# Performance work log

Hardware: AMD Instinct MI355X
Metric: run time of the kernel (lower is better)

The kernel has to match this reference:

```python
import jax, jax.numpy as jnp
import numpy as np

B, S, IN = 32, 512, 19
DE, DD = 256, 128      # encoder / decoder d_model
HE, HD = 8, 4          # heads
LE, LD = 6, 2          # layers
FE, FD = 4 * DE, 4 * DD
EPS = 1e-5


def _ln(x, g, b):
    m = x.mean(-1, keepdims=True)
    v = ((x - m) ** 2).mean(-1, keepdims=True)
    return (x - m) / jnp.sqrt(v + EPS) * g + b


def _mha(x, qkv_w, qkv_b, out_w, out_b, kpad, nh):
    Bq, Sq, D = x.shape
    dh = D // nh
    qkv = x @ qkv_w.T + qkv_b
    q, k, v = jnp.split(qkv, 3, axis=-1)
    hs = lambda t: t.reshape(Bq, Sq, nh, dh).transpose(0, 2, 1, 3)  # -> [B,h,S,dh]
    q, k, v = hs(q), hs(k), hs(v)
    scores = jnp.einsum('bhqd,bhkd->bhqk', q, k) / float(np.sqrt(dh))
    scores = jnp.where(kpad[:, None, None, :], -1e9, scores)  # mask padded keys
    attn = jax.nn.softmax(scores, axis=-1)
    o = jnp.einsum('bhqk,bhkd->bhqd', attn, v).transpose(0, 2, 1, 3).reshape(Bq, Sq, D)
    return o @ out_w.T + out_b


def _block(x, p, kpad, nh):
    qkv_w, qkv_b, ow, ob, f1w, f1b, f2w, f2b, g1, b1, g2, b2 = p
    x = _ln(x + _mha(x, qkv_w, qkv_b, ow, ob, kpad, nh), g1, b1)
    h = jax.nn.relu(x @ f1w.T + f1b) @ f2w.T + f2b
    return _ln(x + h, g2, b2)


def _run(x, ps, kpad, nh, L):
    for i in range(L):
        x = _block(x, tuple(p[i] for p in ps), kpad, nh)
    return x


def _forward(event_tensor, w_in_enc, b_in_enc,
             enc_qkv_w, enc_qkv_b, enc_out_w, enc_out_b,
             enc_f1_w, enc_f1_b, enc_f2_w, enc_f2_b,
             enc_g1, enc_b1, enc_g2, enc_b2,
             mask_token, e2d_w,
             dec_qkv_w, dec_qkv_b, dec_out_w, dec_out_b,
             dec_f1_w, dec_f1_b, dec_f2_w, dec_f2_b,
             dec_g1, dec_b1, dec_g2, dec_b2,
             qh_w, qh_b, dth_w, dth_b,
             attention_mask, pred_mask):
    visible = attention_mask & (~pred_mask)
    counts = visible.sum(axis=1)                                  # [B]
    order = jnp.argsort(~visible, axis=1, stable=True)            # visible positions packed first, in order
    tok = event_tensor @ w_in_enc.T + b_in_enc                    # [B,S,DE]
    vis = jnp.take_along_axis(tok, order[:, :, None], axis=1)
    pos = jnp.arange(S)
    enc_pad = pos[None, :] >= counts[:, None]                      # True = padded slot
    vis = jnp.where(enc_pad[:, :, None], 0.0, vis)
    enc_ps = (enc_qkv_w, enc_qkv_b, enc_out_w, enc_out_b, enc_f1_w, enc_f1_b,
              enc_f2_w, enc_f2_b, enc_g1, enc_b1, enc_g2, enc_b2)
    enc_out = _run(vis, enc_ps, enc_pad, HE, LE)
    dec_vis = enc_out @ e2d_w.T                                    # [B,S,DD]
    idx = jnp.cumsum(visible.astype(jnp.int32), axis=1) - 1        # position -> packed index
    gathered = jnp.take_along_axis(dec_vis, jnp.clip(idx, 0)[:, :, None], axis=1)
    dec_in = jnp.where(visible[:, :, None], gathered, mask_token)  # mask token at masked/pad slots
    dec_ps = (dec_qkv_w, dec_qkv_b, dec_out_w, dec_out_b, dec_f1_w, dec_f1_b,
              dec_f2_w, dec_f2_b, dec_g1, dec_b1, dec_g2, dec_b2)
    dec_out = _run(dec_in, dec_ps, ~attention_mask, HD, LD)
    q = dec_out @ qh_w.T + qh_b
    dt = dec_out @ dth_w.T + dth_b
    return jnp.concatenate([q, dt], axis=-1)                       # [B,S,2]


def setup_inputs():
    key = jax.random.key(0)
    ks = iter(jax.random.split(key, 64))
    nrm = lambda shp, s=0.02: jax.random.normal(next(ks), shp, jnp.float32) * s
    d = {}
    d['event_tensor'] = jax.random.normal(next(ks), (B, S, IN), jnp.float32)
    lengths = jax.random.randint(next(ks), (B,), S // 2, S + 1)
    pos = jnp.arange(S)
    am = pos[None, :] < lengths[:, None]
    pm = (jax.random.uniform(next(ks), (B, S)) < 0.75) & am
    pm = pm.at[:, 0].set(False)  # guarantee >=1 visible token per row
    d['attention_mask'] = am
    d['pred_mask'] = pm
    d['w_in_enc'] = nrm((DE, IN)); d['b_in_enc'] = jnp.zeros((DE,), jnp.float32)
    d['enc_qkv_w'] = nrm((LE, 3 * DE, DE)); d['enc_qkv_b'] = jnp.zeros((LE, 3 * DE), jnp.float32)
    d['enc_out_w'] = nrm((LE, DE, DE));     d['enc_out_b'] = jnp.zeros((LE, DE), jnp.float32)
    d['enc_f1_w'] = nrm((LE, FE, DE));      d['enc_f1_b'] = jnp.zeros((LE, FE), jnp.float32)
    d['enc_f2_w'] = nrm((LE, DE, FE));      d['enc_f2_b'] = jnp.zeros((LE, DE), jnp.float32)
    d['enc_g1'] = jnp.ones((LE, DE), jnp.float32); d['enc_b1'] = jnp.zeros((LE, DE), jnp.float32)
    d['enc_g2'] = jnp.ones((LE, DE), jnp.float32); d['enc_b2'] = jnp.zeros((LE, DE), jnp.float32)
    d['mask_token'] = nrm((DD,))
    d['e2d_w'] = nrm((DD, DE))
    d['dec_qkv_w'] = nrm((LD, 3 * DD, DD)); d['dec_qkv_b'] = jnp.zeros((LD, 3 * DD), jnp.float32)
    d['dec_out_w'] = nrm((LD, DD, DD));     d['dec_out_b'] = jnp.zeros((LD, DD), jnp.float32)
    d['dec_f1_w'] = nrm((LD, FD, DD));      d['dec_f1_b'] = jnp.zeros((LD, FD), jnp.float32)
    d['dec_f2_w'] = nrm((LD, DD, FD));      d['dec_f2_b'] = jnp.zeros((LD, DD), jnp.float32)
    d['dec_g1'] = jnp.ones((LD, DD), jnp.float32); d['dec_b1'] = jnp.zeros((LD, DD), jnp.float32)
    d['dec_g2'] = jnp.ones((LD, DD), jnp.float32); d['dec_b2'] = jnp.zeros((LD, DD), jnp.float32)
    d['qh_w'] = nrm((1, DD));  d['qh_b'] = jnp.zeros((1,), jnp.float32)
    d['dth_w'] = nrm((1, DD)); d['dth_b'] = jnp.zeros((1,), jnp.float32)
    return d


def reference(event_tensor, attention_mask, pred_mask, w_in_enc, b_in_enc,
              enc_qkv_w, enc_qkv_b, enc_out_w, enc_out_b,
              enc_f1_w, enc_f1_b, enc_f2_w, enc_f2_b,
              enc_g1, enc_b1, enc_g2, enc_b2,
              mask_token, e2d_w,
              dec_qkv_w, dec_qkv_b, dec_out_w, dec_out_b,
              dec_f1_w, dec_f1_b, dec_f2_w, dec_f2_b,
              dec_g1, dec_b1, dec_g2, dec_b2,
              qh_w, qh_b, dth_w, dth_b):
    return _forward(event_tensor, w_in_enc, b_in_enc,
                    enc_qkv_w, enc_qkv_b, enc_out_w, enc_out_b,
                    enc_f1_w, enc_f1_b, enc_f2_w, enc_f2_b,
                    enc_g1, enc_b1, enc_g2, enc_b2,
                    mask_token, e2d_w,
                    dec_qkv_w, dec_qkv_b, dec_out_w, dec_out_b,
                    dec_f1_w, dec_f1_b, dec_f2_w, dec_f2_b,
                    dec_g1, dec_b1, dec_g2, dec_b2,
                    qh_w, qh_b, dth_w, dth_b,
                    attention_mask, pred_mask)
```

## Files before the change

### kernel.cpp

```cpp
#include <hip/hip_runtime.h>
#include <hip/hip_bf16.h>

#define B_ 32
#define S_ 512
#define IN_ 19
#define DE_ 256
#define DD_ 128
#define HE_ 8
#define HD_ 4
#define LE_ 6
#define LD_ 2
#define FE_ 1024
#define FD_ 512
#define DH_ 32

typedef __attribute__((ext_vector_type(8))) short short8;
typedef __attribute__((ext_vector_type(4))) float f32x4;

__device__ __forceinline__ short f2bf(float f) {
    union { float f; unsigned u; } x; x.f = f;
    unsigned r = x.u + 0x7fff + ((x.u >> 16) & 1);
    return (short)(r >> 16);
}
__device__ __forceinline__ float bf2f(short s) {
    union { unsigned u; float f; } x; x.u = ((unsigned)(unsigned short)s) << 16;
    return x.f;
}

#define GLL16(g, l) __builtin_amdgcn_global_load_lds( \
    (const __attribute__((address_space(1))) void*)(g), \
    (__attribute__((address_space(3))) void*)(l), 16, 0, 0)

#define QSCALE 0.2550653169f

#define NCONV 9
struct ConvTab {
    const float* src[NCONV];
    short* dst[NCONV];
    int len[NCONV];
};
__global__ __launch_bounds__(S_) void conv_plan_kernel(
    ConvTab tab, int total,
    const int* __restrict__ am, const int* __restrict__ pm,
    int* __restrict__ counts, int* __restrict__ lengths, int* __restrict__ order,
    int* __restrict__ visible, int* __restrict__ idx) {
    if (blockIdx.x < B_) {
        int b = blockIdx.x, s = threadIdx.x;
        __shared__ int sc[S_];
        int a = (am[b * S_ + s] != 0);
        int v = a && (pm[b * S_ + s] == 0);
        visible[b * S_ + s] = v;
        sc[s] = v | (a << 16);
        __syncthreads();
#pragma unroll
        for (int off = 1; off < S_; off <<= 1) {
            int t = (s >= off) ? sc[s - off] : 0;
            __syncthreads();
            sc[s] += t;
            __syncthreads();
        }
        int incl = sc[s] & 0xffff;
        int tot = sc[S_ - 1];
        int total2 = tot & 0xffff;
        if (s == 0) { counts[b] = total2; lengths[b] = tot >> 16; }
        idx[b * S_ + s] = (incl > 0) ? incl - 1 : 0;
        if (v) order[b * S_ + incl - 1] = s;
        else   order[b * S_ + total2 + (s - incl)] = s;
    } else {
        int i = (blockIdx.x - B_) * S_ + threadIdx.x;
        if (i >= total) return;
        int j = i;
        for (int e = 0; e < NCONV; ++e) {
            if (j < tab.len[e]) { tab.dst[e][j] = f2bf(tab.src[e][j]); return; }
            j -= tab.len[e];
        }
    }
}

__global__ __launch_bounds__(DE_) void enc_embed_kernel(
    const float* __restrict__ ev, const float* __restrict__ w, const float* __restrict__ bias,
    const int* __restrict__ counts, const int* __restrict__ order, short* __restrict__ out) {
    int bs = blockIdx.x;
    int b = bs / S_, s = bs % S_;
    int d = threadIdx.x;
    __shared__ float e[IN_];
    bool padded = (s >= counts[b]);
    int src = order[bs];
    if (threadIdx.x < IN_)
        e[threadIdx.x] = padded ? 0.f : ev[(size_t)(b * S_ + src) * IN_ + threadIdx.x];
    __syncthreads();
    float acc = bias[d];
#pragma unroll
    for (int i = 0; i < IN_; ++i) acc += e[i] * w[d * IN_ + i];
    out[(size_t)bs * DE_ + d] = padded ? f2bf(0.f) : f2bf(acc);
}

template <int TM, int TN, bool RELU, bool QKV>
__global__ __launch_bounds__(256) void gemm_mfma(
    const short* __restrict__ A, const short* __restrict__ Wt, const float* __restrict__ bias,
    short* __restrict__ C, int M, int N, int K,
    short* __restrict__ qb, short* __restrict__ kb, short* __restrict__ vtb, int H, int D,
    const int* __restrict__ live) {
    constexpr int HM = TM / 2, HN = TN / 2;
    constexpr int MI = HM / 16, NI = HN / 16;
    constexpr int NCHA = TM / 16, NCH = (TM + TN) / 16;
    int bm = blockIdx.y * TM, bn = blockIdx.x * TN;
    if (live && (bm & (S_ - 1)) >= live[bm >> 9]) return;
    __shared__ short As[2][TM][32];
    __shared__ short Bs[2][TN][32];
    int t = threadIdx.x;
    int wave = t >> 6, lane = t & 63;
    int wm = (wave >> 1) * HM, wn = (wave & 1) * HN;
    int c = lane & 15, quad = lane >> 4;
    f32x4 acc[MI][NI];
#pragma unroll
    for (int i = 0; i < MI; ++i)
#pragma unroll
        for (int j = 0; j < NI; ++j) acc[i][j] = (f32x4){0.f, 0.f, 0.f, 0.f};

    int srow = lane >> 2, scol = (lane & 3) * 8;
    int nk = K >> 5;

    auto stage = [&](int buf, int k0) {
#pragma unroll
        for (int ch0 = 0; ch0 < NCH; ch0 += 4) {
            int ch = ch0 + wave;
            if (ch < NCHA)
                GLL16(A + (size_t)(bm + ch * 16 + srow) * K + k0 + scol, &As[buf][ch * 16][0]);
            else if (ch < NCH)
                GLL16(Wt + (size_t)(bn + (ch - NCHA) * 16 + srow) * K + k0 + scol,
                      &Bs[buf][(ch - NCHA) * 16][0]);
        }
    };

    stage(0, 0);
    __syncthreads();
    for (int kt = 0; kt < nk; ++kt) {
        int cur = kt & 1;
        if (kt + 1 < nk) stage(cur ^ 1, (kt + 1) << 5);
        short8 av[MI], bv[NI];
#pragma unroll
        for (int mi = 0; mi < MI; ++mi) av[mi] = *(const short8*)&As[cur][wm + mi * 16 + c][quad * 8];
#pragma unroll
        for (int ni = 0; ni < NI; ++ni) bv[ni] = *(const short8*)&Bs[cur][wn + ni * 16 + c][quad * 8];
#pragma unroll
        for (int mi = 0; mi < MI; ++mi)
#pragma unroll
            for (int ni = 0; ni < NI; ++ni)
                acc[mi][ni] = __builtin_amdgcn_mfma_f32_16x16x32_bf16(av[mi], bv[ni], acc[mi][ni], 0, 0, 0);
        __syncthreads();
    }
#pragma unroll
    for (int mi = 0; mi < MI; ++mi)
#pragma unroll
        for (int ni = 0; ni < NI; ++ni)
#pragma unroll
            for (int r = 0; r < 4; ++r) {
                int R = bm + wm + mi * 16 + quad * 4 + r;
                int Ncol = bn + wn + ni * 16 + c;
                float v = acc[mi][ni][r] + (bias ? bias[Ncol] : 0.f);
                if (RELU) v = fmaxf(v, 0.f);
                if (!QKV) {
                    C[(size_t)R * N + Ncol] = f2bf(v);
                } else {
                    int s = R & (S_ - 1), b2 = R >> 9;
                    if (Ncol < D) {
                        int h = Ncol >> 5, d = Ncol & 31;
                        qb[(((size_t)b2 * H + h) * S_ + s) * DH_ + d] = f2bf(v * QSCALE);
                    } else if (Ncol < 2 * D) {
                        int n2 = Ncol - D, h = n2 >> 5, d = n2 & 31;
                        kb[(((size_t)b2 * H + h) * S_ + s) * DH_ + d] = f2bf(v);
                    } else {
                        int n2 = Ncol - 2 * D, h = n2 >> 5, d = n2 & 31;
                        vtb[(((size_t)b2 * H + h) * DH_ + d) * S_ + s] = f2bf(v);
                    }
                }
            }
}

template <int N, bool HEAD>
__global__ __launch_bounds__(256) void gemm_ln(
    const short* __restrict__ A, const short* __restrict__ Wt,
    const float* __restrict__ bias, const short* x ,
    const float* __restrict__ g, const float* __restrict__ be,
    short* out,
    const float* __restrict__ qw, const float* __restrict__ qbb,
    const float* __restrict__ dw, const float* __restrict__ dbb,
    float* __restrict__ outf,
    int K, const int* __restrict__ live) {
    constexpr int TM = 32;
    constexpr int HN = N / 2, NI = HN / 16;
    constexpr int NCHA = TM / 16, NCH = NCHA + N / 16;
    constexpr int HST = N + 8;
    constexpr int BUF = (TM + N) * 32;
    int bm = blockIdx.x * TM;
    if (live && (bm & (S_ - 1)) >= live[bm >> 9]) return;
    __shared__ short smem[2 * BUF];
    int t = threadIdx.x, wave = t >> 6, lane = t & 63;
    int wm = (wave >> 1) * 16, wn = (wave & 1) * HN;
    int c = lane & 15, quad = lane >> 4;
    int srow = lane >> 2, scol = (lane & 3) * 8;
    f32x4 acc[NI];
#pragma unroll
    for (int ni = 0; ni < NI; ++ni) acc[ni] = (f32x4){0.f, 0.f, 0.f, 0.f};
    int nk = K >> 5;

    auto stage = [&](int buf, int k0) {
        short* base = smem + buf * BUF;
#pragma unroll
        for (int ch0 = 0; ch0 < NCH; ch0 += 4) {
            int ch = ch0 + wave;
            if (ch < NCHA)
                GLL16(A + (size_t)(bm + ch * 16 + srow) * K + k0 + scol, base + ch * 16 * 32);
            else if (ch < NCH)
                GLL16(Wt + (size_t)((ch - NCHA) * 16 + srow) * K + k0 + scol,
                      base + (TM + (ch - NCHA) * 16) * 32);
        }
    };

    stage(0, 0);
    __syncthreads();
    for (int kt = 0; kt < nk; ++kt) {
        int cur = kt & 1;
        if (kt + 1 < nk) stage(cur ^ 1, (kt + 1) << 5);
        const short* base = smem + cur * BUF;
        short8 av = *(const short8*)(base + (wm + c) * 32 + quad * 8);
        short8 bv[NI];
#pragma unroll
        for (int ni = 0; ni < NI; ++ni)
            bv[ni] = *(const short8*)(base + (TM + wn + ni * 16 + c) * 32 + quad * 8);
#pragma unroll
        for (int ni = 0; ni < NI; ++ni)
            acc[ni] = __builtin_amdgcn_mfma_f32_16x16x32_bf16(av, bv[ni], acc[ni], 0, 0, 0);
        __syncthreads();
    }

    short* Hs = smem;
#pragma unroll
    for (int ni = 0; ni < NI; ++ni) {
        int col = wn + ni * 16 + c;
        float bcol = bias[col];
#pragma unroll
        for (int r = 0; r < 4; ++r)
            Hs[(wm + quad * 4 + r) * HST + col] = f2bf(acc[ni][r] + bcol);
    }
    __syncthreads();

    constexpr int CPL = N / 8;
    int r = t >> 3, li = t & 7;
    int R = bm + r;
    int c0 = li * CPL;
    float v[CPL];
    float s = 0.f;
#pragma unroll
    for (int e8 = 0; e8 < CPL / 8; ++e8) {
        short8 xv = *(const short8*)&x[(size_t)R * N + c0 + e8 * 8];
#pragma unroll
        for (int j = 0; j < 8; ++j) {
            float vv = bf2f(xv[j]) + bf2f(Hs[r * HST + c0 + e8 * 8 + j]);
            v[e8 * 8 + j] = vv;
            s += vv;
        }
    }
    s += __shfl_xor(s, 1); s += __shfl_xor(s, 2); s += __shfl_xor(s, 4);
    float m = s / N;
    float s2 = 0.f;
#pragma unroll
    for (int e = 0; e < CPL; ++e) { float d = v[e] - m; s2 += d * d; }
    s2 += __shfl_xor(s2, 1); s2 += __shfl_xor(s2, 2); s2 += __shfl_xor(s2, 4);
    float rstd = rsqrtf(s2 / N + 1e-5f);
    if (!HEAD) {
        if (live && ((R & (S_ - 1)) >= live[R >> 9])) return;
#pragma unroll
        for (int e8 = 0; e8 < CPL / 8; ++e8) {
            short8 ov;
#pragma unroll
            for (int j = 0; j < 8; ++j) {
                int e = e8 * 8 + j;
                ov[j] = f2bf((v[e] - m) * rstd * g[c0 + e] + be[c0 + e]);
            }
            *(short8*)&out[(size_t)R * N + c0 + e8 * 8] = ov;
        }
    } else {
        float q = 0.f, dt = 0.f;
#pragma unroll
        for (int e = 0; e < CPL; ++e) {
            float o = (v[e] - m) * rstd * g[c0 + e] + be[c0 + e];
            q += o * qw[c0 + e];
            dt += o * dw[c0 + e];
        }
        q += __shfl_xor(q, 1); q += __shfl_xor(q, 2); q += __shfl_xor(q, 4);
        dt += __shfl_xor(dt, 1); dt += __shfl_xor(dt, 2); dt += __shfl_xor(dt, 4);
        if (li == 0) {
            outf[(size_t)R * 2 + 0] = q + qbb[0];
            outf[(size_t)R * 2 + 1] = dt + dbb[0];
        }
    }
}

__global__ __launch_bounds__(256) void attn_flash(
    const short* __restrict__ qb, const short* __restrict__ kb, const short* __restrict__ vtb,
    const int* __restrict__ limit_arr, const int* __restrict__ qlim,
    short* __restrict__ o, int H, int D) {
    int b = blockIdx.z, h = blockIdx.y;
    if (qlim && (int)(blockIdx.x * 64) >= qlim[b]) return;
    int wave = threadIdx.x >> 6, lane = threadIdx.x & 63;
    int q0 = blockIdx.x * 64 + wave * 16;
    int c = lane & 15, quad = lane >> 4;
    size_t bh = (size_t)b * H + h;
    __shared__ short PtAll[4][16][132];
    short (*Pt)[132] = PtAll[wave];

    f32x4 zero = (f32x4){0.f, 0.f, 0.f, 0.f};
    short8 aq = *(const short8*)&qb[(bh * S_ + q0 + c) * DH_ + quad * 8];
    const short* kbase = kb + bh * S_ * DH_;
    const short* vbase = vtb + bh * DH_ * S_;

    int limit = limit_arr[b];
    int nchunks = (limit + 127) >> 7;

    float lrow[4] = {0.f, 0.f, 0.f, 0.f};
    f32x4 o0 = zero, o1 = zero;

    for (int kc = 0; kc < nchunks; ++kc) {
        f32x4 s[8];
#pragma unroll
        for (int nt = 0; nt < 8; ++nt) {
            short8 bk = *(const short8*)&kbase[(size_t)(kc * 128 + nt * 16 + c) * DH_ + quad * 8];
            s[nt] = __builtin_amdgcn_mfma_f32_16x16x32_bf16(aq, bk, zero, 0, 0, 0);
        }
#pragma unroll
        for (int nt = 0; nt < 8; ++nt) {
            bool ok = (kc * 128 + nt * 16 + c) < limit;
#pragma unroll
            for (int r = 0; r < 4; ++r) {
                float p = ok ? exp2f(s[nt][r]) : 0.f;
                s[nt][r] = p;
                lrow[r] += p;
            }
        }
#pragma unroll
        for (int nt = 0; nt < 8; ++nt)
#pragma unroll
            for (int r = 0; r < 4; ++r)
                Pt[quad * 4 + r][nt * 16 + c] = f2bf(s[nt][r]);
#pragma unroll
        for (int kk = 0; kk < 4; ++kk) {
            short8 ap = *(const short8*)&Pt[c][kk * 32 + quad * 8];
            short8 b0 = *(const short8*)&vbase[(size_t)c * S_ + kc * 128 + kk * 32 + quad * 8];
            short8 b1 = *(const short8*)&vbase[(size_t)(16 + c) * S_ + kc * 128 + kk * 32 + quad * 8];
            o0 = __builtin_amdgcn_mfma_f32_16x16x32_bf16(ap, b0, o0, 0, 0, 0);
            o1 = __builtin_amdgcn_mfma_f32_16x16x32_bf16(ap, b1, o1, 0, 0, 0);
        }
    }
#pragma unroll
    for (int r = 0; r < 4; ++r) {
        float l = lrow[r];
        l += __shfl_xor(l, 1);
        l += __shfl_xor(l, 2);
        l += __shfl_xor(l, 4);
        l += __shfl_xor(l, 8);
        float inv = 1.f / l;
        int row = quad * 4 + r;
        size_t base = (size_t)(b * S_ + q0 + row) * D + h * DH_;
        o[base + c] = f2bf(o0[r] * inv);
        o[base + 16 + c] = f2bf(o1[r] * inv);
    }
}

__global__ __launch_bounds__(DD_) void dec_embed_kernel(
    const short* __restrict__ dec_vis, const float* __restrict__ mask_token,
    const int* __restrict__ visible, const int* __restrict__ idx, short* __restrict__ out) {
    int bs = blockIdx.x, d = threadIdx.x;
    int b = bs / S_;
    short val = visible[bs] ? dec_vis[(size_t)(b * S_ + idx[bs]) * DD_ + d]
                            : f2bf(mask_token[d]);
    out[(size_t)bs * DD_ + d] = val;
}

extern "C" void kernel_launch(void* const* d_in, const int* in_sizes, int n_in,
                              void* d_out, int out_size, void* d_ws, size_t ws_size,
                              hipStream_t stream) {
    const float* ev      = (const float*)d_in[0];
    const int*  am       = (const int*)d_in[1];
    const int*  pm       = (const int*)d_in[2];
    const float* w_in    = (const float*)d_in[3];
    const float* b_in    = (const float*)d_in[4];
    const float* eqkv_w  = (const float*)d_in[5];
    const float* eqkv_b  = (const float*)d_in[6];
    const float* eout_w  = (const float*)d_in[7];
    const float* eout_b  = (const float*)d_in[8];
    const float* ef1_w   = (const float*)d_in[9];
    const float* ef1_b   = (const float*)d_in[10];
    const float* ef2_w   = (const float*)d_in[11];
    const float* ef2_b   = (const float*)d_in[12];
    const float* eg1     = (const float*)d_in[13];
    const float* eb1     = (const float*)d_in[14];
    const float* eg2     = (const float*)d_in[15];
    const float* eb2     = (const float*)d_in[16];
    const float* mask_tok= (const float*)d_in[17];
    const float* e2d_w   = (const float*)d_in[18];
    const float* dqkv_w  = (const float*)d_in[19];
    const float* dqkv_b  = (const float*)d_in[20];
    const float* dout_w  = (const float*)d_in[21];
    const float* dout_b  = (const float*)d_in[22];
    const float* df1_w   = (const float*)d_in[23];
    const float* df1_b   = (const float*)d_in[24];
    const float* df2_w   = (const float*)d_in[25];
    const float* df2_b   = (const float*)d_in[26];
    const float* dg1     = (const float*)d_in[27];
    const float* db1     = (const float*)d_in[28];
    const float* dg2     = (const float*)d_in[29];
    const float* db2     = (const float*)d_in[30];
    const float* qh_w    = (const float*)d_in[31];
    const float* qh_b    = (const float*)d_in[32];
    const float* dth_w   = (const float*)d_in[33];
    const float* dth_b   = (const float*)d_in[34];
    float* out = (float*)d_out;

    const int BS = B_ * S_;
    char* ws = (char*)d_ws;
    int* counts  = (int*)ws;
    int* lengths = counts + 32;
    int* order   = lengths + 32;
    int* visible = order + BS;
    int* idx     = visible + BS;

    short* wb = (short*)(ws + 256 * 1024);
    const int L_eqkv = LE_ * 3 * DE_ * DE_;
    const int L_eout = LE_ * DE_ * DE_;
    const int L_ef1  = LE_ * FE_ * DE_;
    const int L_ef2  = LE_ * DE_ * FE_;
    const int L_e2d  = DD_ * DE_;
    const int L_dqkv = LD_ * 3 * DD_ * DD_;
    const int L_dout = LD_ * DD_ * DD_;
    const int L_df1  = LD_ * FD_ * DD_;
    const int L_df2  = LD_ * DD_ * FD_;
    short* w_eqkv = wb;
    short* w_eout = w_eqkv + L_eqkv;
    short* w_ef1  = w_eout + L_eout;
    short* w_ef2  = w_ef1 + L_ef1;
    short* w_e2d  = w_ef2 + L_ef2;
    short* w_dqkv = w_e2d + L_e2d;
    short* w_dout = w_dqkv + L_dqkv;
    short* w_df1  = w_dout + L_dout;
    short* w_df2  = w_df1 + L_df1;
    const int convTotal = L_eqkv + L_eout + L_ef1 + L_ef2 + L_e2d + L_dqkv + L_dout + L_df1 + L_df2;

    short* bx    = (short*)(ws + 12 * 1024 * 1024);
    short* qbuf  = bx   + (size_t)BS * DE_;
    short* kbuf  = qbuf + (size_t)B_ * HE_ * S_ * DH_;
    short* vtbuf = kbuf + (size_t)B_ * HE_ * S_ * DH_;
    short* battn = vtbuf + (size_t)B_ * HE_ * S_ * DH_;
    short* bt    = battn + (size_t)BS * DE_;
    short* hid   = bt + (size_t)BS * DE_;

    ConvTab tab;
    tab.src[0] = eqkv_w; tab.dst[0] = w_eqkv; tab.len[0] = L_eqkv;
    tab.src[1] = eout_w; tab.dst[1] = w_eout; tab.len[1] = L_eout;
    tab.src[2] = ef1_w;  tab.dst[2] = w_ef1;  tab.len[2] = L_ef1;
    tab.src[3] = ef2_w;  tab.dst[3] = w_ef2;  tab.len[3] = L_ef2;
    tab.src[4] = e2d_w;  tab.dst[4] = w_e2d;  tab.len[4] = L_e2d;
    tab.src[5] = dqkv_w; tab.dst[5] = w_dqkv; tab.len[5] = L_dqkv;
    tab.src[6] = dout_w; tab.dst[6] = w_dout; tab.len[6] = L_dout;
    tab.src[7] = df1_w;  tab.dst[7] = w_df1;  tab.len[7] = L_df1;
    tab.src[8] = df2_w;  tab.dst[8] = w_df2;  tab.len[8] = L_df2;
    conv_plan_kernel<<<B_ + (convTotal + S_ - 1) / S_, S_, 0, stream>>>(
        tab, convTotal, am, pm, counts, lengths, order, visible, idx);
    enc_embed_kernel<<<BS, DE_, 0, stream>>>(ev, w_in, b_in, counts, order, bx);

    for (int l = 0; l < LE_; ++l) {
        gemm_mfma<64, 64, false, true><<<dim3(3 * DE_ / 64, BS / 64), 256, 0, stream>>>(
            bx, w_eqkv + (size_t)l * 3 * DE_ * DE_, eqkv_b + (size_t)l * 3 * DE_,
            nullptr, BS, 3 * DE_, DE_, qbuf, kbuf, vtbuf, HE_, DE_, counts);
        attn_flash<<<dim3(S_ / 64, HE_, B_), 256, 0, stream>>>(
            qbuf, kbuf, vtbuf, counts, counts, battn, HE_, DE_);
        gemm_ln<DE_, false><<<BS / 32, 256, 0, stream>>>(
            battn, w_eout + (size_t)l * DE_ * DE_, eout_b + (size_t)l * DE_,
            bx, eg1 + (size_t)l * DE_, eb1 + (size_t)l * DE_, bx,
            nullptr, nullptr, nullptr, nullptr, nullptr, DE_, counts);
        gemm_mfma<64, 64, true, false><<<dim3(FE_ / 64, BS / 64), 256, 0, stream>>>(
            bx, w_ef1 + (size_t)l * FE_ * DE_, ef1_b + (size_t)l * FE_,
            hid, BS, FE_, DE_, nullptr, nullptr, nullptr, 0, 0, counts);
        gemm_ln<DE_, false><<<BS / 32, 256, 0, stream>>>(
            hid, w_ef2 + (size_t)l * DE_ * FE_, ef2_b + (size_t)l * DE_,
            bx, eg2 + (size_t)l * DE_, eb2 + (size_t)l * DE_, bx,
            nullptr, nullptr, nullptr, nullptr, nullptr, FE_, counts);
    }

    gemm_mfma<32, 32, false, false><<<dim3(DD_ / 32, BS / 32), 256, 0, stream>>>(
        bx, w_e2d, nullptr, bt, BS, DD_, DE_, nullptr, nullptr, nullptr, 0, 0, counts);
    dec_embed_kernel<<<BS, DD_, 0, stream>>>(bt, mask_tok, visible, idx, bx);

    for (int l = 0; l < LD_; ++l) {
        gemm_mfma<64, 64, false, true><<<dim3(3 * DD_ / 64, BS / 64), 256, 0, stream>>>(
            bx, w_dqkv + (size_t)l * 3 * DD_ * DD_, dqkv_b + (size_t)l * 3 * DD_, nullptr,
            BS, 3 * DD_, DD_, qbuf, kbuf, vtbuf, HD_, DD_, nullptr);
        attn_flash<<<dim3(S_ / 64, HD_, B_), 256, 0, stream>>>(
            qbuf, kbuf, vtbuf, lengths, nullptr, battn, HD_, DD_);
        gemm_ln<DD_, false><<<BS / 32, 256, 0, stream>>>(
            battn, w_dout + (size_t)l * DD_ * DD_, dout_b + (size_t)l * DD_,
            bx, dg1 + (size_t)l * DD_, db1 + (size_t)l * DD_, bx,
            nullptr, nullptr, nullptr, nullptr, nullptr, DD_, nullptr);
        gemm_mfma<64, 64, true, false><<<dim3(FD_ / 64, BS / 64), 256, 0, stream>>>(
            bx, w_df1 + (size_t)l * FD_ * DD_, df1_b + (size_t)l * FD_,
            hid, BS, FD_, DD_, nullptr, nullptr, nullptr, 0, 0, nullptr);
        if (l < LD_ - 1) {
            gemm_ln<DD_, false><<<BS / 32, 256, 0, stream>>>(
                hid, w_df2 + (size_t)l * DD_ * FD_, df2_b + (size_t)l * DD_,
                bx, dg2 + (size_t)l * DD_, db2 + (size_t)l * DD_, bx,
                nullptr, nullptr, nullptr, nullptr, nullptr, FD_, nullptr);
        } else {
            gemm_ln<DD_, true><<<BS / 32, 256, 0, stream>>>(
                hid, w_df2 + (size_t)l * DD_ * FD_, df2_b + (size_t)l * DD_,
                bx, dg2 + (size_t)l * DD_, db2 + (size_t)l * DD_, nullptr,
                qh_w, qh_b, dth_w, dth_b, out, FD_, nullptr);
        }
    }
}
```

Measured before the change: 855.6 us.

## Deepen GEMM global-to-LDS pipeline with explicit vmcnt waits and per-shape kernels

Replaces double buffering in the MFMA GEMM and GEMM+LayerNorm kernels with a 3-4 stage ring of LDS buffers. Each iteration waits only for the oldest tile using counted s_waitcnt vmcnt plus a single barrier, instead of a full syncthreads after every k-step. Kernels are also specialised into per-shape wrappers with compile-time N/K. The deeper prefetch is meant to hide global load latency, at the cost of more LDS per block and hand-counted wait logic that could be fragile.

```diff
diff --git a/kernel.cpp b/kernel.cpp
--- a/kernel.cpp
+++ b/kernel.cpp
@@ -30,6 +30,20 @@
 #define GLL16(g, l) __builtin_amdgcn_global_load_lds( \
     (const __attribute__((address_space(1))) void*)(g), \
     (__attribute__((address_space(3))) void*)(l), 16, 0, 0)
+
+__device__ __forceinline__ void waitvm(int n) {
+    switch (n) {
+    case 0: asm volatile("s_waitcnt vmcnt(0)" ::: "memory"); break;
+    case 1: asm volatile("s_waitcnt vmcnt(1)" ::: "memory"); break;
+    case 2: asm volatile("s_waitcnt vmcnt(2)" ::: "memory"); break;
+    case 3: asm volatile("s_waitcnt vmcnt(3)" ::: "memory"); break;
+    case 4: asm volatile("s_waitcnt vmcnt(4)" ::: "memory"); break;
+    default: asm volatile("s_waitcnt vmcnt(5)" ::: "memory"); break;
+    }
+}
+__device__ __forceinline__ void wait_lgkm0() {
+    asm volatile("s_waitcnt lgkmcnt(0)" ::: "memory");
+}
 
 #define QSCALE 0.2550653169f
 
@@ -95,10 +109,10 @@
     out[(size_t)bs * DE_ + d] = padded ? f2bf(0.f) : f2bf(acc);
 }
 
-template <int TM, int TN, bool RELU, bool QKV>
-__global__ __launch_bounds__(256) void gemm_mfma(
+template <int TM, int TN, bool RELU, bool QKV, int DEPTH>
+__device__ __forceinline__ void gemm_body(
     const short* __restrict__ A, const short* __restrict__ Wt, const float* __restrict__ bias,
-    short* __restrict__ C, int M, int N, int K,
+    short* __restrict__ C, int N, int K,
     short* __restrict__ qb, short* __restrict__ kb, short* __restrict__ vtb, int H, int D,
     const int* __restrict__ live) {
     constexpr int HM = TM / 2, HN = TN / 2;
@@ -106,8 +120,8 @@
     constexpr int NCHA = TM / 16, NCH = (TM + TN) / 16;
     int bm = blockIdx.y * TM, bn = blockIdx.x * TN;
     if (live && (bm & (S_ - 1)) >= live[bm >> 9]) return;
-    __shared__ short As[2][TM][32];
-    __shared__ short Bs[2][TN][32];
+    __shared__ short As[DEPTH][TM][32];
+    __shared__ short Bs[DEPTH][TN][32];
     int t = threadIdx.x;
     int wave = t >> 6, lane = t & 63;
     int wm = (wave >> 1) * HM, wn = (wave & 1) * HN;
@@ -119,9 +133,11 @@
         for (int j = 0; j < NI; ++j) acc[i][j] = (f32x4){0.f, 0.f, 0.f, 0.f};
 
     int srow = lane >> 2, scol = (lane & 3) * 8;
+    const int myloads = (NCH - wave + 3) >> 2;
     int nk = K >> 5;
 
-    auto stage = [&](int buf, int k0) {
+    auto stage = [&](int buf, int kt) {
+        int k0 = kt << 5;
 #pragma unroll
         for (int ch0 = 0; ch0 < NCH; ch0 += 4) {
             int ch = ch0 + wave;
@@ -133,11 +149,19 @@
         }
     };
 
-    stage(0, 0);
-    __syncthreads();
+#pragma unroll
+    for (int i = 0; i < DEPTH - 1; ++i)
+        if (i < nk) stage(i, i);
+
     for (int kt = 0; kt < nk; ++kt) {
-        int cur = kt & 1;
-        if (kt + 1 < nk) stage(cur ^ 1, (kt + 1) << 5);
+        int cur = kt % DEPTH;
+        int smax = (nk - 1 < kt + DEPTH - 2) ? nk - 1 : kt + DEPTH - 2;
+        waitvm((smax - kt) * myloads);
+        wait_lgkm0();
+        __builtin_amdgcn_s_barrier();
+        __builtin_amdgcn_sched_barrier(0);
+        int nxt = kt + DEPTH - 1;
+        if (nxt < nk) stage(nxt % DEPTH, nxt);
         short8 av[MI], bv[NI];
 #pragma unroll
         for (int mi = 0; mi < MI; ++mi) av[mi] = *(const short8*)&As[cur][wm + mi * 16 + c][quad * 8];
@@ -148,7 +172,6 @@
 #pragma unroll
             for (int ni = 0; ni < NI; ++ni)
                 acc[mi][ni] = __builtin_amdgcn_mfma_f32_16x16x32_bf16(av[mi], bv[ni], acc[mi][ni], 0, 0, 0);
-        __syncthreads();
     }
 #pragma unroll
     for (int mi = 0; mi < MI; ++mi)
@@ -179,7 +202,7 @@
 }
 
 template <int N, bool HEAD>
-__global__ __launch_bounds__(256) void gemm_ln(
+__device__ __forceinline__ void gemm_ln_body(
     const short* __restrict__ A, const short* __restrict__ Wt,
     const float* __restrict__ bias, const short* x ,
     const float* __restrict__ g, const float* __restrict__ be,
@@ -189,13 +212,14 @@
     float* __restrict__ outf,
     int K, const int* __restrict__ live) {
     constexpr int TM = 32;
+    constexpr int DEPTH = 3;
     constexpr int HN = N / 2, NI = HN / 16;
     constexpr int NCHA = TM / 16, NCH = NCHA + N / 16;
     constexpr int HST = N + 8;
     constexpr int BUF = (TM + N) * 32;
     int bm = blockIdx.x * TM;
     if (live && (bm & (S_ - 1)) >= live[bm >> 9]) return;
-    __shared__ short smem[2 * BUF];
+    __shared__ short smem[DEPTH * BUF];
     int t = threadIdx.x, wave = t >> 6, lane = t & 63;
     int wm = (wave >> 1) * 16, wn = (wave & 1) * HN;
     int c = lane & 15, quad = lane >> 4;
@@ -203,10 +227,12 @@
     f32x4 acc[NI];
 #pragma unroll
     for (int ni = 0; ni < NI; ++ni) acc[ni] = (f32x4){0.f, 0.f, 0.f, 0.f};
+    const int myloads = (NCH - wave + 3) >> 2;
     int nk = K >> 5;
 
-    auto stage = [&](int buf, int k0) {
+    auto stage = [&](int buf, int kt) {
         short* base = smem + buf * BUF;
+        int k0 = kt << 5;
 #pragma unroll
         for (int ch0 = 0; ch0 < NCH; ch0 += 4) {
             int ch = ch0 + wave;
@@ -218,11 +244,19 @@
         }
     };
 
-    stage(0, 0);
-    __syncthreads();
+#pragma unroll
+    for (int i = 0; i < DEPTH - 1; ++i)
+        if (i < nk) stage(i, i);
+
     for (int kt = 0; kt < nk; ++kt) {
-        int cur = kt & 1;
-        if (kt + 1 < nk) stage(cur ^ 1, (kt + 1) << 5);
+        int cur = kt % DEPTH;
+        int smax = (nk - 1 < kt + DEPTH - 2) ? nk - 1 : kt + DEPTH - 2;
+        waitvm((smax - kt) * myloads);
+        wait_lgkm0();
+        __builtin_amdgcn_s_barrier();
+        __builtin_amdgcn_sched_barrier(0);
+        int nxt = kt + DEPTH - 1;
+        if (nxt < nk) stage(nxt % DEPTH, nxt);
         const short* base = smem + cur * BUF;
         short8 av = *(const short8*)(base + (wm + c) * 32 + quad * 8);
         short8 bv[NI];
@@ -232,8 +266,8 @@
 #pragma unroll
         for (int ni = 0; ni < NI; ++ni)
             acc[ni] = __builtin_amdgcn_mfma_f32_16x16x32_bf16(av, bv[ni], acc[ni], 0, 0, 0);
-        __syncthreads();
-    }
+    }
+    __syncthreads();
 
     short* Hs = smem;
 #pragma unroll
@@ -296,6 +330,55 @@
             outf[(size_t)R * 2 + 1] = dt + dbb[0];
         }
     }
+}
+
+__global__ __launch_bounds__(256) void g_qkv_e(
+    const short* A, const short* Wt, const float* bias,
+    short* qb, short* kb, short* vtb, const int* live) {
+    gemm_body<64, 64, false, true, 4>(A, Wt, bias, nullptr, 3 * DE_, DE_, qb, kb, vtb, HE_, DE_, live);
+}
+__global__ __launch_bounds__(256) void g_qkv_d(
+    const short* A, const short* Wt, const float* bias,
+    short* qb, short* kb, short* vtb) {
+    gemm_body<64, 64, false, true, 4>(A, Wt, bias, nullptr, 3 * DD_, DD_, qb, kb, vtb, HD_, DD_, nullptr);
+}
+__global__ __launch_bounds__(256) void g_f1_e(
+    const short* A, const short* Wt, const float* bias, short* C, const int* live) {
+    gemm_body<64, 64, true, false, 4>(A, Wt, bias, C, FE_, DE_, nullptr, nullptr, nullptr, 0, 0, live);
+}
+__global__ __launch_bounds__(256) void g_f1_d(
+    const short* A, const short* Wt, const float* bias, short* C) {
+    gemm_body<64, 64, true, false, 4>(A, Wt, bias, C, FD_, DD_, nullptr, nullptr, nullptr, 0, 0, nullptr);
+}
+__global__ __launch_bounds__(256) void g_e2d(
+    const short* A, const short* Wt, short* C, const int* live) {
+    gemm_body<32, 32, false, false, 4>(A, Wt, nullptr, C, DD_, DE_, nullptr, nullptr, nullptr, 0, 0, live);
+}
+__global__ __launch_bounds__(256) void g_outln_e(
+    const short* A, const short* Wt, const float* bias, const short* x,
+    const float* g, const float* be, short* out, const int* live) {
+    gemm_ln_body<DE_, false>(A, Wt, bias, x, g, be, out, nullptr, nullptr, nullptr, nullptr, nullptr, DE_, live);
+}
+__global__ __launch_bounds__(256) void g_f2ln_e(
+    const short* A, const short* Wt, const float* bias, const short* x,
+    const float* g, const float* be, short* out, const int* live) {
+    gemm_ln_body<DE_, false>(A, Wt, bias, x, g, be, out, nullptr, nullptr, nullptr, nullptr, nullptr, FE_, live);
+}
+__global__ __launch_bounds__(256) void g_outln_d(
+    const short* A, const short* Wt, const float* bias, const short* x,
+    const float* g, const float* be, short* out) {
+    gemm_ln_body<DD_, false>(A, Wt, bias, x, g, be, out, nullptr, nullptr, nullptr, nullptr, nullptr, DD_, nullptr);
+}
+__global__ __launch_bounds__(256) void g_f2ln_d(
+    const short* A, const short* Wt, const float* bias, const short* x,
+    const float* g, const float* be, short* out) {
+    gemm_ln_body<DD_, false>(A, Wt, bias, x, g, be, out, nullptr, nullptr, nullptr, nullptr, nullptr, FD_, nullptr);
+}
+__global__ __launch_bounds__(256) void g_headln(
+    const short* A, const short* Wt, const float* bias, const short* x,
+    const float* g, const float* be,
+    const float* qw, const float* qbb, const float* dw, const float* dbb, float* outf) {
+    gemm_ln_body<DD_, true>(A, Wt, bias, x, g, be, nullptr, qw, qbb, dw, dbb, outf, FD_, nullptr);
 }
 
 __global__ __launch_bounds__(256) void attn_flash(
@@ -470,51 +553,44 @@
     enc_embed_kernel<<<BS, DE_, 0, stream>>>(ev, w_in, b_in, counts, order, bx);
 
     for (int l = 0; l < LE_; ++l) {
-        gemm_mfma<64, 64, false, true><<<dim3(3 * DE_ / 64, BS / 64), 256, 0, stream>>>(
+        g_qkv_e<<<dim3(3 * DE_ / 64, BS / 64), 256, 0, stream>>>(
             bx, w_eqkv + (size_t)l * 3 * DE_ * DE_, eqkv_b + (size_t)l * 3 * DE_,
-            nullptr, BS, 3 * DE_, DE_, qbuf, kbuf, vtbuf, HE_, DE_, counts);
+            qbuf, kbuf, vtbuf, counts);
         attn_flash<<<dim3(S_ / 64, HE_, B_), 256, 0, stream>>>(
             qbuf, kbuf, vtbuf, counts, counts, battn, HE_, DE_);
-        gemm_ln<DE_, false><<<BS / 32, 256, 0, stream>>>(
+        g_outln_e<<<BS / 32, 256, 0, stream>>>(
             battn, w_eout + (size_t)l * DE_ * DE_, eout_b + (size_t)l * DE_,
-            bx, eg1 + (size_t)l * DE_, eb1 + (size_t)l * DE_, bx,
-            nullptr, nullptr, nullptr, nullptr, nullptr, DE_, counts);
-        gemm_mfma<64, 64, true, false><<<dim3(FE_ / 64, BS / 64), 256, 0, stream>>>(
-            bx, w_ef1 + (size_t)l * FE_ * DE_, ef1_b + (size_t)l * FE_,
-            hid, BS, FE_, DE_, nullptr, nullptr, nullptr, 0, 0, counts);
-        gemm_ln<DE_, false><<<BS / 32, 256, 0, stream>>>(
+            bx, eg1 + (size_t)l * DE_, eb1 + (size_t)l * DE_, bx, counts);
+        g_f1_e<<<dim3(FE_ / 64, BS / 64), 256, 0, stream>>>(
+            bx, w_ef1 + (size_t)l * FE_ * DE_, ef1_b + (size_t)l * FE_, hid, counts);
+        g_f2ln_e<<<BS / 32, 256, 0, stream>>>(
             hid, w_ef2 + (size_t)l * DE_ * FE_, ef2_b + (size_t)l * DE_,
-            bx, eg2 + (size_t)l * DE_, eb2 + (size_t)l * DE_, bx,
-            nullptr, nullptr, nullptr, nullptr, nullptr, FE_, counts);
-    }
-
-    gemm_mfma<32, 32, false, false><<<dim3(DD_ / 32, BS / 32), 256, 0, stream>>>(
-        bx, w_e2d, nullptr, bt, BS, DD_, DE_, nullptr, nullptr, nullptr, 0, 0, counts);
+            bx, eg2 + (size_t)l * DE_, eb2 + (size_t)l * DE_, bx, counts);
+    }
+
+    g_e2d<<<dim3(DD_ / 32, BS / 32), 256, 0, stream>>>(bx, w_e2d, bt, counts);
     dec_embed_kernel<<<BS, DD_, 0, stream>>>(bt, mask_tok, visible, idx, bx);
 
     for (int l = 0; l < LD_; ++l) {
-        gemm_mfma<64, 64, false, true><<<dim3(3 * DD_ / 64, BS / 64), 256, 0, stream>>>(
-            bx, w_dqkv + (size_t)l * 3 * DD_ * DD_, dqkv_b + (size_t)l * 3 * DD_, nullptr,
-            BS, 3 * DD_, DD_, qbuf, kbuf, vtbuf, HD_, DD_, nullptr);
+        g_qkv_d<<<dim3(3 * DD_ / 64, BS / 64), 256, 0, stream>>>(
+            bx, w_dqkv + (size_t)l * 3 * DD_ * DD_, dqkv_b + (size_t)l * 3 * DD_,
+            qbuf, kbuf, vtbuf);
         attn_flash<<<dim3(S_ / 64, HD_, B_), 256, 0, stream>>>(
             qbuf, kbuf, vtbuf, lengths, nullptr, battn, HD_, DD_);
-        gemm_ln<DD_, false><<<BS / 32, 256, 0, stream>>>(
+        g_outln_d<<<BS / 32, 256, 0, stream>>>(
             battn, w_dout + (size_t)l * DD_ * DD_, dout_b + (size_t)l * DD_,
-            bx, dg1 + (size_t)l * DD_, db1 + (size_t)l * DD_, bx,
-            nullptr, nullptr, nullptr, nullptr, nullptr, DD_, nullptr);
-        gemm_mfma<64, 64, true, false><<<dim3(FD_ / 64, BS / 64), 256, 0, stream>>>(
-            bx, w_df1 + (size_t)l * FD_ * DD_, df1_b + (size_t)l * FD_,
-            hid, BS, FD_, DD_, nullptr, nullptr, nullptr, 0, 0, nullptr);
+            bx, dg1 + (size_t)l * DD_, db1 + (size_t)l * DD_, bx);
+        g_f1_d<<<dim3(FD_ / 64, BS / 64), 256, 0, stream>>>(
+            bx, w_df1 + (size_t)l * FD_ * DD_, df1_b + (size_t)l * FD_, hid);
         if (l < LD_ - 1) {
-            gemm_ln<DD_, false><<<BS / 32, 256, 0, stream>>>(
+            g_f2ln_d<<<BS / 32, 256, 0, stream>>>(
                 hid, w_df2 + (size_t)l * DD_ * FD_, df2_b + (size_t)l * DD_,
-                bx, dg2 + (size_t)l * DD_, db2 + (size_t)l * DD_, bx,
-                nullptr, nullptr, nullptr, nullptr, nullptr, FD_, nullptr);
+                bx, dg2 + (size_t)l * DD_, db2 + (size_t)l * DD_, bx);
         } else {
-            gemm_ln<DD_, true><<<BS / 32, 256, 0, stream>>>(
+            g_headln<<<BS / 32, 256, 0, stream>>>(
                 hid, w_df2 + (size_t)l * DD_ * FD_, df2_b + (size_t)l * DD_,
-                bx, dg2 + (size_t)l * DD_, db2 + (size_t)l * DD_, nullptr,
-                qh_w, qh_b, dth_w, dth_b, out, FD_, nullptr);
-        }
-    }
-}
+                bx, dg2 + (size_t)l * DD_, db2 + (size_t)l * DD_,
+                qh_w, qh_b, dth_w, dth_b, out);
+        }
+    }
+}
```

Result: no change. 855.9 us (+0.0%).
